# Performance work log

Measured on AMD Instinct MI355X. Metric: run time of the kernel, lower is better.

Reference implementation:

```python
import jax, jax.numpy as jnp
import numpy as np

# 8 voxel corner offsets in {0,1}^3 (order matches signed offsets in the
# torch module after the *0.5+0.5 remap used inside splitting/trilinear calls)
_CORNERS = np.array([[1,1,1],[1,1,0],[1,0,1],[0,1,1],[1,0,0],[0,1,0],[0,0,1],[0,0,0]], dtype=np.float32)

K = 150000   # unique corner keys (embedding rows)
V = 100000   # voxels
N = 262144   # query samples (rays * steps)
D = 64       # quantized_embed_dim


def setup_inputs() -> dict:
    key = jax.random.key(0)
    k1, k2, k3, k4, k5 = jax.random.split(key, 5)
    values = jax.random.normal(k1, (K, D), dtype=jnp.float32)
    p = jax.random.uniform(k2, (N, 3), dtype=jnp.float32)            # local trilinear coords in [0,1]
    W_proj = jax.random.normal(k3, (D, D), dtype=jnp.float32) / np.sqrt(D)
    b_proj = jnp.zeros((D,), dtype=jnp.float32)
    feats = jax.random.randint(k4, (V, 8), 0, K, dtype=jnp.int64) if jax.config.read('jax_enable_x64') else jax.random.randint(k4, (V, 8), 0, K).astype(jnp.int32)
    sample_vidx = jax.random.randint(k5, (N,), 0, V).astype(jnp.int32)
    return {"values": values, "p": p, "W_proj": W_proj, "b_proj": b_proj,
            "feats": feats, "sample_vidx": sample_vidx}


def trilinear_interp(p, q, corner_feats):
    # p: [N,3] in [0,1]; q: [8,3] corners in {0,1}; corner_feats: [N,8,D]
    # weight per corner = prod_d (p*q + (1-p)*(1-q))  -- identical to NSVF trilinear_interp
    w = jnp.prod(p[:, None, :] * q[None] + (1.0 - p[:, None, :]) * (1.0 - q[None]), axis=-1)  # [N,8]
    return jnp.einsum('nc,ncd->nd', w, corner_feats)


def reference(values, p, W_proj, b_proj, feats, sample_vidx):
    q = jnp.asarray(_CORNERS)
    corner_idx = feats[sample_vidx]          # [N,8] irregular gather of corner keys
    corner_feats = values[corner_idx]        # [N,8,D] embedding gather
    feat = trilinear_interp(p, q, corner_feats)   # [N,D]
    out = feat @ W_proj + b_proj             # values_proj Linear(embed_dim, embed_dim)
    return out
```

## Files before the change

kernel.cpp:

```cpp
#include <hip/hip_runtime.h>

#define TPB 256

typedef __attribute__((ext_vector_type(8))) short bf16x8;
typedef __attribute__((ext_vector_type(4))) float f32x4;

__device__ __forceinline__ unsigned pack_bf16_rne(float lo, float hi) {
    union { float f; unsigned u; } a, b;
    a.f = lo; b.f = hi;
    unsigned ua = (a.u + 0x7fffu + ((a.u >> 16) & 1u)) >> 16;
    unsigned ub = (b.u + 0x7fffu + ((b.u >> 16) & 1u)) >> 16;
    return ua | (ub << 16);
}
__device__ __forceinline__ float bf_lo(unsigned u) {
    union { unsigned i; float f; } c; c.i = u << 16; return c.f;
}
__device__ __forceinline__ float bf_hi(unsigned u) {
    union { unsigned i; float f; } c; c.i = u & 0xffff0000u; return c.f;
}

__global__ __launch_bounds__(TPB) void cvt_values_bf16(
    const float4* __restrict__ src, uint4* __restrict__ dst, int n8)
{
    int i = blockIdx.x * TPB + threadIdx.x;
    if (i < n8) {
        const float4 a = src[2 * i];
        const float4 b = src[2 * i + 1];
        uint4 o;
        o.x = pack_bf16_rne(a.x, a.y);
        o.y = pack_bf16_rne(a.z, a.w);
        o.z = pack_bf16_rne(b.x, b.y);
        o.w = pack_bf16_rne(b.z, b.w);
        dst[i] = o;
    }
}

__global__ void cvt_w_frag(const float* __restrict__ W, uint4* __restrict__ wfrag)
{
    const int t = threadIdx.x;
    for (int e = t; e < 512; e += TPB) {
        const int l  = e & 63;
        const int f  = e >> 6;
        const int ct = f >> 1;
        const int kf = f & 1;
        const int col = ct * 16 + (l & 15);
        const int k0  = kf * 32 + 8 * (l >> 4);
        uint4 o;
        o.x = pack_bf16_rne(W[(k0 + 0) * 64 + col], W[(k0 + 1) * 64 + col]);
        o.y = pack_bf16_rne(W[(k0 + 2) * 64 + col], W[(k0 + 3) * 64 + col]);
        o.z = pack_bf16_rne(W[(k0 + 4) * 64 + col], W[(k0 + 5) * 64 + col]);
        o.w = pack_bf16_rne(W[(k0 + 6) * 64 + col], W[(k0 + 7) * 64 + col]);
        wfrag[e] = o;
    }
}

__global__ __launch_bounds__(TPB) void fused_embed_proj_mfma(
    const unsigned* __restrict__ valbf,
    const float* __restrict__ p,
    const uint4* __restrict__ wfrag,
    const float* __restrict__ b,
    const int*   __restrict__ feats,
    const int*   __restrict__ vidx,
    float* __restrict__ out,
    int N)
{
    __shared__ float featS[64][68];

    const int t    = threadIdx.x;
    const int base = blockIdx.x * 64;
    const int g8   = t & 7;
    const int si   = t >> 3;

    int   cidx[2][8];
    float wgt[2][8];
    #pragma unroll
    for (int i = 0; i < 2; ++i) {
        const int s = si + 32 * i;
        int n = base + s;
        if (n >= N) n = N - 1;

        const int v = vidx[n];
        const int4 f0 = *(const int4*)&feats[(size_t)v * 8];
        const int4 f1 = *(const int4*)&feats[(size_t)v * 8 + 4];
        cidx[i][0] = f0.x; cidx[i][1] = f0.y; cidx[i][2] = f0.z; cidx[i][3] = f0.w;
        cidx[i][4] = f1.x; cidx[i][5] = f1.y; cidx[i][6] = f1.z; cidx[i][7] = f1.w;

        const float px = p[n * 3 + 0];
        const float py = p[n * 3 + 1];
        const float pz = p[n * 3 + 2];
        const float ox = 1.0f - px, oy = 1.0f - py, oz = 1.0f - pz;
        wgt[i][0] = px * py * pz;
        wgt[i][1] = px * py * oz;
        wgt[i][2] = px * oy * pz;
        wgt[i][3] = ox * py * pz;
        wgt[i][4] = px * oy * oz;
        wgt[i][5] = ox * py * oz;
        wgt[i][6] = ox * oy * pz;
        wgt[i][7] = ox * oy * oz;
    }

    #pragma unroll
    for (int i = 0; i < 2; ++i) {
        float a0 = 0.f, a1 = 0.f, a2 = 0.f, a3 = 0.f;
        float a4 = 0.f, a5 = 0.f, a6 = 0.f, a7 = 0.f;
        #pragma unroll
        for (int c = 0; c < 8; ++c) {
            const uint4 q = *(const uint4*)&valbf[(size_t)cidx[i][c] * 32 + 4 * g8];
            const float w = wgt[i][c];
            a0 = fmaf(w, bf_lo(q.x), a0);
            a1 = fmaf(w, bf_hi(q.x), a1);
            a2 = fmaf(w, bf_lo(q.y), a2);
            a3 = fmaf(w, bf_hi(q.y), a3);
            a4 = fmaf(w, bf_lo(q.z), a4);
            a5 = fmaf(w, bf_hi(q.z), a5);
            a6 = fmaf(w, bf_lo(q.w), a6);
            a7 = fmaf(w, bf_hi(q.w), a7);
        }
        const int s  = si + 32 * i;
        const int pc = ((g8 + s) & 7) << 3;
        float4 lo; lo.x = a0; lo.y = a1; lo.z = a2; lo.w = a3;
        float4 hi; hi.x = a4; hi.y = a5; hi.z = a6; hi.w = a7;
        *(float4*)&featS[s][pc]     = lo;
        *(float4*)&featS[s][pc + 4] = hi;
    }

    const int l = t & 63;
    const int w = t >> 6;
    uint4 wf[8];
    #pragma unroll
    for (int f = 0; f < 8; ++f) wf[f] = wfrag[f * 64 + l];
    float bias[4];
    #pragma unroll
    for (int ct = 0; ct < 4; ++ct) bias[ct] = b[ct * 16 + (l & 15)];

    __syncthreads();

    const int arow = 16 * w + (l & 15);
    const int kg   = l >> 4;

    bf16x8 afrag[2];
    #pragma unroll
    for (int kf = 0; kf < 2; ++kf) {
        const int bk = 4 * kf + kg;
        const int pc = ((bk + arow) & 7) << 3;
        const float4 x0 = *(const float4*)&featS[arow][pc];
        const float4 x1 = *(const float4*)&featS[arow][pc + 4];
        union { unsigned u[4]; bf16x8 v; } cvt;
        cvt.u[0] = pack_bf16_rne(x0.x, x0.y);
        cvt.u[1] = pack_bf16_rne(x0.z, x0.w);
        cvt.u[2] = pack_bf16_rne(x1.x, x1.y);
        cvt.u[3] = pack_bf16_rne(x1.z, x1.w);
        afrag[kf] = cvt.v;
    }

    #pragma unroll
    for (int ct = 0; ct < 4; ++ct) {
        f32x4 acc;
        acc[0] = bias[ct]; acc[1] = bias[ct]; acc[2] = bias[ct]; acc[3] = bias[ct];
        union { uint4 u; bf16x8 v; } b0, b1;
        b0.u = wf[ct * 2 + 0];
        b1.u = wf[ct * 2 + 1];
        acc = __builtin_amdgcn_mfma_f32_16x16x32_bf16(afrag[0], b0.v, acc, 0, 0, 0);
        acc = __builtin_amdgcn_mfma_f32_16x16x32_bf16(afrag[1], b1.v, acc, 0, 0, 0);

        const int col = ct * 16 + (l & 15);
        #pragma unroll
        for (int r = 0; r < 4; ++r) {
            const int n = base + 16 * w + kg * 4 + r;
            if (n < N) out[(size_t)n * 64 + col] = acc[r];
        }
    }
}

__global__ __launch_bounds__(TPB) void fused_embed_proj_fp32(
    const float* __restrict__ values, const float* __restrict__ p,
    const float* __restrict__ W, const float* __restrict__ b,
    const int* __restrict__ feats, const int* __restrict__ vidx,
    float* __restrict__ out, int N)
{
    __shared__ float featS[64][68];
    __shared__ float Wlds[64][64];

    const int t    = threadIdx.x;
    const int base = blockIdx.x * 64;
    {
        const float4* Wv = (const float4*)W;
        float4*       Wl = (float4*)&Wlds[0][0];
        #pragma unroll
        for (int i = 0; i < 4; ++i) Wl[t + i * TPB] = Wv[t + i * TPB];
    }
    const int g  = t & 15;
    const int sb = t >> 4;

    int   cidx[4][8];
    float wgt[4][8];
    #pragma unroll
    for (int i = 0; i < 4; ++i) {
        const int s = sb + 16 * i;
        int n = base + s;
        if (n >= N) n = N - 1;
        const int v = vidx[n];
        const int4 f0 = *(const int4*)&feats[(size_t)v * 8];
        const int4 f1 = *(const int4*)&feats[(size_t)v * 8 + 4];
        cidx[i][0] = f0.x; cidx[i][1] = f0.y; cidx[i][2] = f0.z; cidx[i][3] = f0.w;
        cidx[i][4] = f1.x; cidx[i][5] = f1.y; cidx[i][6] = f1.z; cidx[i][7] = f1.w;
        const float px = p[n * 3], py = p[n * 3 + 1], pz = p[n * 3 + 2];
        const float ox = 1.f - px, oy = 1.f - py, oz = 1.f - pz;
        wgt[i][0] = px * py * pz; wgt[i][1] = px * py * oz;
        wgt[i][2] = px * oy * pz; wgt[i][3] = ox * py * pz;
        wgt[i][4] = px * oy * oz; wgt[i][5] = ox * py * oz;
        wgt[i][6] = ox * oy * pz; wgt[i][7] = ox * oy * oz;
    }
    #pragma unroll
    for (int i = 0; i < 4; ++i) {
        float4 acc; acc.x = acc.y = acc.z = acc.w = 0.f;
        #pragma unroll
        for (int c = 0; c < 8; ++c) {
            const float4 val = *(const float4*)&values[(size_t)cidx[i][c] * 64 + 4 * g];
            const float w = wgt[i][c];
            acc.x = fmaf(w, val.x, acc.x); acc.y = fmaf(w, val.y, acc.y);
            acc.z = fmaf(w, val.z, acc.z); acc.w = fmaf(w, val.w, acc.w);
        }
        *(float4*)&featS[sb + 16 * i][4 * g] = acc;
    }
    __syncthreads();

    const int tx = t & 15, ty = t >> 4;
    float acc[4][4];
    {
        const float4 bb = ((const float4*)b)[tx];
        #pragma unroll
        for (int j = 0; j < 4; ++j) {
            acc[j][0] = bb.x; acc[j][1] = bb.y; acc[j][2] = bb.z; acc[j][3] = bb.w;
        }
    }
    #pragma unroll 4
    for (int d = 0; d < 64; ++d) {
        const float a0 = featS[4 * ty + 0][d];
        const float a1 = featS[4 * ty + 1][d];
        const float a2 = featS[4 * ty + 2][d];
        const float a3 = featS[4 * ty + 3][d];
        const float4 wr = *(const float4*)&Wlds[d][4 * tx];
        acc[0][0] = fmaf(a0, wr.x, acc[0][0]); acc[0][1] = fmaf(a0, wr.y, acc[0][1]);
        acc[0][2] = fmaf(a0, wr.z, acc[0][2]); acc[0][3] = fmaf(a0, wr.w, acc[0][3]);
        acc[1][0] = fmaf(a1, wr.x, acc[1][0]); acc[1][1] = fmaf(a1, wr.y, acc[1][1]);
        acc[1][2] = fmaf(a1, wr.z, acc[1][2]); acc[1][3] = fmaf(a1, wr.w, acc[1][3]);
        acc[2][0] = fmaf(a2, wr.x, acc[2][0]); acc[2][1] = fmaf(a2, wr.y, acc[2][1]);
        acc[2][2] = fmaf(a2, wr.z, acc[2][2]); acc[2][3] = fmaf(a2, wr.w, acc[2][3]);
        acc[3][0] = fmaf(a3, wr.x, acc[3][0]); acc[3][1] = fmaf(a3, wr.y, acc[3][1]);
        acc[3][2] = fmaf(a3, wr.z, acc[3][2]); acc[3][3] = fmaf(a3, wr.w, acc[3][3]);
    }
    #pragma unroll
    for (int j = 0; j < 4; ++j) {
        const int n = base + 4 * ty + j;
        if (n < N) {
            float4 o; o.x = acc[j][0]; o.y = acc[j][1]; o.z = acc[j][2]; o.w = acc[j][3];
            *(float4*)&out[(size_t)n * 64 + 4 * tx] = o;
        }
    }
}

extern "C" void kernel_launch(void* const* d_in, const int* in_sizes, int n_in,
                              void* d_out, int out_size, void* d_ws, size_t ws_size,
                              hipStream_t stream) {
    const float* values = (const float*)d_in[0];
    const float* p      = (const float*)d_in[1];
    const float* W      = (const float*)d_in[2];
    const float* b      = (const float*)d_in[3];
    const int*   feats  = (const int*)d_in[4];
    const int*   vidx   = (const int*)d_in[5];
    float* out = (float*)d_out;

    const int N  = in_sizes[5];
    const int KD = in_sizes[0];
    const int nblocks = (N + 63) / 64;

    const size_t val_bytes = (size_t)KD * 2;
    const size_t need      = val_bytes + 8192;
    if (ws_size >= need) {
        unsigned* valbf = (unsigned*)d_ws;
        uint4*    wfrag = (uint4*)((char*)d_ws + val_bytes);
        const int n8 = KD / 8;
        cvt_values_bf16<<<(n8 + TPB - 1) / TPB, TPB, 0, stream>>>(
            (const float4*)values, (uint4*)valbf, n8);
        cvt_w_frag<<<1, TPB, 0, stream>>>(W, wfrag);
        fused_embed_proj_mfma<<<nblocks, TPB, 0, stream>>>(
            valbf, p, wfrag, b, feats, vidx, out, N);
    } else {
        fused_embed_proj_fp32<<<nblocks, TPB, 0, stream>>>(
            values, p, W, b, feats, vidx, out, N);
    }
}
```

Measured before the change: 71.39 us.

## Merge conversion kernels and compute MFMA A-fragments directly in registers

The two preprocessing kernels (values to bf16 and W to MFMA fragments) become one launch, with the last block handling W. The main kernel drops the LDS staging and barrier: each lane gathers the exact K slices its MFMA A-fragment needs and packs them straight to bf16. Output stores become nontemporal. This removes one launch, the shared-memory round trip and the sync, at the cost of different gather coalescing (two 16-byte loads per corner per lane) and W fragment loads from global inside the MFMA loop.

```diff
diff --git a/kernel.cpp b/kernel.cpp
--- a/kernel.cpp
+++ b/kernel.cpp
@@ -19,10 +19,29 @@
     union { unsigned i; float f; } c; c.i = u & 0xffff0000u; return c.f;
 }
 
-__global__ __launch_bounds__(TPB) void cvt_values_bf16(
-    const float4* __restrict__ src, uint4* __restrict__ dst, int n8)
+__global__ __launch_bounds__(TPB) void cvt_inputs(
+    const float4* __restrict__ src, uint4* __restrict__ dst, int n8,
+    const float* __restrict__ W, uint4* __restrict__ wfrag, int nvb)
 {
-    int i = blockIdx.x * TPB + threadIdx.x;
+    if ((int)blockIdx.x == nvb) {
+        const int t = threadIdx.x;
+        for (int e = t; e < 512; e += TPB) {
+            const int l  = e & 63;
+            const int f  = e >> 6;
+            const int ct = f >> 1;
+            const int kf = f & 1;
+            const int col = ct * 16 + (l & 15);
+            const int k0  = kf * 32 + 8 * (l >> 4);
+            uint4 o;
+            o.x = pack_bf16_rne(W[(k0 + 0) * 64 + col], W[(k0 + 1) * 64 + col]);
+            o.y = pack_bf16_rne(W[(k0 + 2) * 64 + col], W[(k0 + 3) * 64 + col]);
+            o.z = pack_bf16_rne(W[(k0 + 4) * 64 + col], W[(k0 + 5) * 64 + col]);
+            o.w = pack_bf16_rne(W[(k0 + 6) * 64 + col], W[(k0 + 7) * 64 + col]);
+            wfrag[e] = o;
+        }
+        return;
+    }
+    const int i = blockIdx.x * TPB + threadIdx.x;
     if (i < n8) {
         const float4 a = src[2 * i];
         const float4 b = src[2 * i + 1];
@@ -32,25 +51,6 @@
         o.z = pack_bf16_rne(b.x, b.y);
         o.w = pack_bf16_rne(b.z, b.w);
         dst[i] = o;
-    }
-}
-
-__global__ void cvt_w_frag(const float* __restrict__ W, uint4* __restrict__ wfrag)
-{
-    const int t = threadIdx.x;
-    for (int e = t; e < 512; e += TPB) {
-        const int l  = e & 63;
-        const int f  = e >> 6;
-        const int ct = f >> 1;
-        const int kf = f & 1;
-        const int col = ct * 16 + (l & 15);
-        const int k0  = kf * 32 + 8 * (l >> 4);
-        uint4 o;
-        o.x = pack_bf16_rne(W[(k0 + 0) * 64 + col], W[(k0 + 1) * 64 + col]);
-        o.y = pack_bf16_rne(W[(k0 + 2) * 64 + col], W[(k0 + 3) * 64 + col]);
-        o.z = pack_bf16_rne(W[(k0 + 4) * 64 + col], W[(k0 + 5) * 64 + col]);
-        o.w = pack_bf16_rne(W[(k0 + 6) * 64 + col], W[(k0 + 7) * 64 + col]);
-        wfrag[e] = o;
     }
 }
 
@@ -64,110 +64,95 @@
     float* __restrict__ out,
     int N)
 {
-    __shared__ float featS[64][68];
-
     const int t    = threadIdx.x;
-    const int base = blockIdx.x * 64;
-    const int g8   = t & 7;
-    const int si   = t >> 3;
-
-    int   cidx[2][8];
-    float wgt[2][8];
-    #pragma unroll
-    for (int i = 0; i < 2; ++i) {
-        const int s = si + 32 * i;
-        int n = base + s;
-        if (n >= N) n = N - 1;
-
-        const int v = vidx[n];
-        const int4 f0 = *(const int4*)&feats[(size_t)v * 8];
-        const int4 f1 = *(const int4*)&feats[(size_t)v * 8 + 4];
-        cidx[i][0] = f0.x; cidx[i][1] = f0.y; cidx[i][2] = f0.z; cidx[i][3] = f0.w;
-        cidx[i][4] = f1.x; cidx[i][5] = f1.y; cidx[i][6] = f1.z; cidx[i][7] = f1.w;
-
-        const float px = p[n * 3 + 0];
-        const float py = p[n * 3 + 1];
-        const float pz = p[n * 3 + 2];
-        const float ox = 1.0f - px, oy = 1.0f - py, oz = 1.0f - pz;
-        wgt[i][0] = px * py * pz;
-        wgt[i][1] = px * py * oz;
-        wgt[i][2] = px * oy * pz;
-        wgt[i][3] = ox * py * pz;
-        wgt[i][4] = px * oy * oz;
-        wgt[i][5] = ox * py * oz;
-        wgt[i][6] = ox * oy * pz;
-        wgt[i][7] = ox * oy * oz;
-    }
-
-    #pragma unroll
-    for (int i = 0; i < 2; ++i) {
-        float a0 = 0.f, a1 = 0.f, a2 = 0.f, a3 = 0.f;
-        float a4 = 0.f, a5 = 0.f, a6 = 0.f, a7 = 0.f;
-        #pragma unroll
-        for (int c = 0; c < 8; ++c) {
-            const uint4 q = *(const uint4*)&valbf[(size_t)cidx[i][c] * 32 + 4 * g8];
-            const float w = wgt[i][c];
-            a0 = fmaf(w, bf_lo(q.x), a0);
-            a1 = fmaf(w, bf_hi(q.x), a1);
-            a2 = fmaf(w, bf_lo(q.y), a2);
-            a3 = fmaf(w, bf_hi(q.y), a3);
-            a4 = fmaf(w, bf_lo(q.z), a4);
-            a5 = fmaf(w, bf_hi(q.z), a5);
-            a6 = fmaf(w, bf_lo(q.w), a6);
-            a7 = fmaf(w, bf_hi(q.w), a7);
-        }
-        const int s  = si + 32 * i;
-        const int pc = ((g8 + s) & 7) << 3;
-        float4 lo; lo.x = a0; lo.y = a1; lo.z = a2; lo.w = a3;
-        float4 hi; hi.x = a4; hi.y = a5; hi.z = a6; hi.w = a7;
-        *(float4*)&featS[s][pc]     = lo;
-        *(float4*)&featS[s][pc + 4] = hi;
-    }
-
-    const int l = t & 63;
-    const int w = t >> 6;
-    uint4 wf[8];
-    #pragma unroll
-    for (int f = 0; f < 8; ++f) wf[f] = wfrag[f * 64 + l];
-    float bias[4];
-    #pragma unroll
-    for (int ct = 0; ct < 4; ++ct) bias[ct] = b[ct * 16 + (l & 15)];
-
-    __syncthreads();
-
-    const int arow = 16 * w + (l & 15);
-    const int kg   = l >> 4;
-
-    bf16x8 afrag[2];
-    #pragma unroll
-    for (int kf = 0; kf < 2; ++kf) {
-        const int bk = 4 * kf + kg;
-        const int pc = ((bk + arow) & 7) << 3;
-        const float4 x0 = *(const float4*)&featS[arow][pc];
-        const float4 x1 = *(const float4*)&featS[arow][pc + 4];
-        union { unsigned u[4]; bf16x8 v; } cvt;
-        cvt.u[0] = pack_bf16_rne(x0.x, x0.y);
-        cvt.u[1] = pack_bf16_rne(x0.z, x0.w);
-        cvt.u[2] = pack_bf16_rne(x1.x, x1.y);
-        cvt.u[3] = pack_bf16_rne(x1.z, x1.w);
-        afrag[kf] = cvt.v;
+    const int l    = t & 63;
+    const int w    = t >> 6;
+    const int base = blockIdx.x * 64 + 16 * w;
+    const int srow = l & 15;
+    const int kq   = l >> 4;
+
+    int n = base + srow;
+    if (n >= N) n = N - 1;
+
+    const int v = vidx[n];
+    const int4 f0 = *(const int4*)&feats[(size_t)v * 8];
+    const int4 f1 = *(const int4*)&feats[(size_t)v * 8 + 4];
+    const int c0 = f0.x, c1 = f0.y, c2 = f0.z, c3 = f0.w;
+    const int c4 = f1.x, c5 = f1.y, c6 = f1.z, c7 = f1.w;
+
+    const float px = p[n * 3 + 0];
+    const float py = p[n * 3 + 1];
+    const float pz = p[n * 3 + 2];
+    const float ox = 1.0f - px, oy = 1.0f - py, oz = 1.0f - pz;
+    float wgt[8];
+    wgt[0] = px * py * pz;
+    wgt[1] = px * py * oz;
+    wgt[2] = px * oy * pz;
+    wgt[3] = ox * py * pz;
+    wgt[4] = px * oy * oz;
+    wgt[5] = ox * py * oz;
+    wgt[6] = ox * oy * pz;
+    wgt[7] = ox * oy * oz;
+    int cidx[8] = {c0, c1, c2, c3, c4, c5, c6, c7};
+
+    float a0[8] = {0.f,0.f,0.f,0.f,0.f,0.f,0.f,0.f};
+    float a1[8] = {0.f,0.f,0.f,0.f,0.f,0.f,0.f,0.f};
+    #pragma unroll
+    for (int c = 0; c < 8; ++c) {
+        const unsigned* row = valbf + (size_t)cidx[c] * 32;
+        const uint4 q0 = *(const uint4*)(row + 4 * kq);
+        const uint4 q1 = *(const uint4*)(row + 16 + 4 * kq);
+        const float wc = wgt[c];
+        a0[0] = fmaf(wc, bf_lo(q0.x), a0[0]);
+        a0[1] = fmaf(wc, bf_hi(q0.x), a0[1]);
+        a0[2] = fmaf(wc, bf_lo(q0.y), a0[2]);
+        a0[3] = fmaf(wc, bf_hi(q0.y), a0[3]);
+        a0[4] = fmaf(wc, bf_lo(q0.z), a0[4]);
+        a0[5] = fmaf(wc, bf_hi(q0.z), a0[5]);
+        a0[6] = fmaf(wc, bf_lo(q0.w), a0[6]);
+        a0[7] = fmaf(wc, bf_hi(q0.w), a0[7]);
+        a1[0] = fmaf(wc, bf_lo(q1.x), a1[0]);
+        a1[1] = fmaf(wc, bf_hi(q1.x), a1[1]);
+        a1[2] = fmaf(wc, bf_lo(q1.y), a1[2]);
+        a1[3] = fmaf(wc, bf_hi(q1.y), a1[3]);
+        a1[4] = fmaf(wc, bf_lo(q1.z), a1[4]);
+        a1[5] = fmaf(wc, bf_hi(q1.z), a1[5]);
+        a1[6] = fmaf(wc, bf_lo(q1.w), a1[6]);
+        a1[7] = fmaf(wc, bf_hi(q1.w), a1[7]);
+    }
+
+    bf16x8 afrag0, afrag1;
+    {
+        union { unsigned u[4]; bf16x8 v; } cv;
+        cv.u[0] = pack_bf16_rne(a0[0], a0[1]);
+        cv.u[1] = pack_bf16_rne(a0[2], a0[3]);
+        cv.u[2] = pack_bf16_rne(a0[4], a0[5]);
+        cv.u[3] = pack_bf16_rne(a0[6], a0[7]);
+        afrag0 = cv.v;
+        cv.u[0] = pack_bf16_rne(a1[0], a1[1]);
+        cv.u[1] = pack_bf16_rne(a1[2], a1[3]);
+        cv.u[2] = pack_bf16_rne(a1[4], a1[5]);
+        cv.u[3] = pack_bf16_rne(a1[6], a1[7]);
+        afrag1 = cv.v;
     }
 
     #pragma unroll
     for (int ct = 0; ct < 4; ++ct) {
+        const float bias = b[ct * 16 + srow];
         f32x4 acc;
-        acc[0] = bias[ct]; acc[1] = bias[ct]; acc[2] = bias[ct]; acc[3] = bias[ct];
+        acc[0] = bias; acc[1] = bias; acc[2] = bias; acc[3] = bias;
         union { uint4 u; bf16x8 v; } b0, b1;
-        b0.u = wf[ct * 2 + 0];
-        b1.u = wf[ct * 2 + 1];
-        acc = __builtin_amdgcn_mfma_f32_16x16x32_bf16(afrag[0], b0.v, acc, 0, 0, 0);
-        acc = __builtin_amdgcn_mfma_f32_16x16x32_bf16(afrag[1], b1.v, acc, 0, 0, 0);
-
-        const int col = ct * 16 + (l & 15);
+        b0.u = wfrag[(ct * 2 + 0) * 64 + l];
+        b1.u = wfrag[(ct * 2 + 1) * 64 + l];
+        acc = __builtin_amdgcn_mfma_f32_16x16x32_bf16(afrag0, b0.v, acc, 0, 0, 0);
+        acc = __builtin_amdgcn_mfma_f32_16x16x32_bf16(afrag1, b1.v, acc, 0, 0, 0);
+
+        const int col = ct * 16 + srow;
         #pragma unroll
         for (int r = 0; r < 4; ++r) {
-            const int n = base + 16 * w + kg * 4 + r;
-            if (n < N) out[(size_t)n * 64 + col] = acc[r];
+            const int n2 = base + 4 * kq + r;
+            if (n2 < N)
+                __builtin_nontemporal_store(acc[r], &out[(size_t)n2 * 64 + col]);
         }
     }
 }
@@ -280,10 +265,10 @@
     if (ws_size >= need) {
         unsigned* valbf = (unsigned*)d_ws;
         uint4*    wfrag = (uint4*)((char*)d_ws + val_bytes);
-        const int n8 = KD / 8;
-        cvt_values_bf16<<<(n8 + TPB - 1) / TPB, TPB, 0, stream>>>(
-            (const float4*)values, (uint4*)valbf, n8);
-        cvt_w_frag<<<1, TPB, 0, stream>>>(W, wfrag);
+        const int n8  = KD / 8;
+        const int nvb = (n8 + TPB - 1) / TPB;
+        cvt_inputs<<<nvb + 1, TPB, 0, stream>>>(
+            (const float4*)values, (uint4*)valbf, n8, W, wfrag, nvb);
         fused_embed_proj_mfma<<<nblocks, TPB, 0, stream>>>(
             valbf, p, wfrag, b, feats, vidx, out, N);
     } else {
```

After: 69.76 us. 1.02x faster.
